# Optimization experiments

Hardware: AMD Instinct MI355X
Metric: run time of the kernel (lower is better)

## Reference

```python
import jax, jax.numpy as jnp
import numpy as np

N_NODES = 100000
N_EDGES = 3200000
N_GRAPHS = 64
F_IN = 64
NUM_CLASSES = 10
CHROM = 21


def _glorot(key, shape):
    fan_in, fan_out = shape
    lim = (6.0 / (fan_in + fan_out)) ** 0.5
    return jax.random.uniform(key, shape, jnp.float32, -lim, lim)


def setup_inputs() -> dict:
    key = jax.random.key(0)
    ks = jax.random.split(key, 16)
    x = jax.random.normal(ks[0], (N_NODES, F_IN), jnp.float32)
    edge_index = jax.random.randint(ks[1], (2, N_EDGES), 0, N_NODES, jnp.int32)
    batch = jnp.sort(jax.random.randint(ks[2], (N_NODES,), 0, N_GRAPHS, jnp.int32))
    return {
        "x": x,
        "edge_index": edge_index,
        "batch": batch,
        # SAGEConv1: 64 -> 16
        "W1l": _glorot(ks[3], (F_IN, 16)), "b1": jnp.zeros((16,), jnp.float32),
        "W1r": _glorot(ks[4], (F_IN, 16)),
        # SAGEConv2: 16 -> 32
        "W2l": _glorot(ks[5], (16, 32)), "b2": jnp.zeros((32,), jnp.float32),
        "W2r": _glorot(ks[6], (16, 32)),
        # SAGEConv3: 32 -> 21
        "W3l": _glorot(ks[7], (32, CHROM)), "b3": jnp.zeros((CHROM,), jnp.float32),
        "W3r": _glorot(ks[8], (32, CHROM)),
        # classifier: 32 -> num_classes
        "Wc": _glorot(ks[9], (32, NUM_CLASSES)), "bc": jnp.zeros((NUM_CLASSES,), jnp.float32),
    }


def _sage_conv(x, src, dst, Wl, b, Wr):
    # mean aggregation of source features at target nodes (PyG SAGEConv default)
    agg = jax.ops.segment_sum(x[src], dst, num_segments=N_NODES)
    cnt = jax.ops.segment_sum(jnp.ones((src.shape[0],), x.dtype), dst, num_segments=N_NODES)
    mean = agg / jnp.maximum(cnt, 1.0)[:, None]
    return mean @ Wl + b + x @ Wr


def reference(x, edge_index, batch, W1l, b1, W1r, W2l, b2, W2r, W3l, b3, W3r, Wc, bc):
    src, dst = edge_index[0], edge_index[1]
    h = jax.nn.relu(_sage_conv(x, src, dst, W1l, b1, W1r))
    h2 = _sage_conv(h, src, dst, W2l, b2, W2r)          # pooled pre-relu
    color = _sage_conv(jax.nn.relu(h2), src, dst, W3l, b3, W3r)
    # global_mean_pool over graphs
    gsum = jax.ops.segment_sum(h2, batch, num_segments=N_GRAPHS)
    gcnt = jax.ops.segment_sum(jnp.ones((h2.shape[0],), h2.dtype), batch, num_segments=N_GRAPHS)
    pooled = gsum / jnp.maximum(gcnt, 1.0)[:, None]
    # dropout p=0.3 is identity in eval mode
    classif = pooled @ Wc + bc
    return classif, color
```

## Files before the change

### kernel.cpp

```cpp
#include <hip/hip_runtime.h>
#include <hip/hip_fp16.h>
#include <cstdint>
#include <cstddef>

#define N_NODES  100000
#define N_EDGES  3200000
#define N_GRAPHS 64

#define BQBITS   9
#define BQ       512
#define NBUCK    196
#define TILE     4096
#define NBLK     782
#define POOL_SLICES 8
#define PADB     4608


__global__ void kp1_hist(const int* __restrict__ dst, int* __restrict__ gh, int ne) {
    __shared__ int h[NBUCK];
    for (int i = threadIdx.x; i < NBUCK; i += 256) h[i] = 0;
    __syncthreads();
    int base = blockIdx.x * TILE;
    for (int i = threadIdx.x; i < TILE; i += 256) {
        int e = base + i;
        if (e < ne) atomicAdd(&h[dst[e] >> BQBITS], 1);
    }
    __syncthreads();
    for (int i = threadIdx.x; i < NBUCK; i += 256) gh[i * NBLK + blockIdx.x] = h[i];
}

__global__ void kp1_scanA(int* __restrict__ gh, int* __restrict__ btotal) {
    int q = blockIdx.x;
    __shared__ int ts[256];
    int v[4];
    int tsum = 0;
#pragma unroll
    for (int u = 0; u < 4; ++u) {
        int idx = threadIdx.x * 4 + u;
        v[u] = (idx < NBLK) ? gh[q * NBLK + idx] : 0;
        tsum += v[u];
    }
    ts[threadIdx.x] = tsum;
    __syncthreads();
    for (int off = 1; off < 256; off <<= 1) {
        int t = (threadIdx.x >= off) ? ts[threadIdx.x - off] : 0;
        __syncthreads();
        ts[threadIdx.x] += t;
        __syncthreads();
    }
    int run = ts[threadIdx.x] - tsum;
#pragma unroll
    for (int u = 0; u < 4; ++u) {
        int idx = threadIdx.x * 4 + u;
        if (idx < NBLK) gh[q * NBLK + idx] = run;
        run += v[u];
    }
    if (threadIdx.x == 255) btotal[q] = ts[255];
}

__global__ void kp1_scanB(const int* __restrict__ btotal, int* __restrict__ bstart) {
    __shared__ int s[256];
    int v = (threadIdx.x < NBUCK) ? btotal[threadIdx.x] : 0;
    s[threadIdx.x] = v;
    __syncthreads();
    for (int off = 1; off < 256; off <<= 1) {
        int t = (threadIdx.x >= off) ? s[threadIdx.x - off] : 0;
        __syncthreads();
        s[threadIdx.x] += t;
        __syncthreads();
    }
    if (threadIdx.x < NBUCK) bstart[threadIdx.x] = s[threadIdx.x] - v;
    if (threadIdx.x == 0) bstart[NBUCK] = N_EDGES;
}

__global__ __launch_bounds__(256) void kp1_scatter(
        const int* __restrict__ src, const int* __restrict__ dst,
        const int* __restrict__ gh, const int* __restrict__ bstart,
        unsigned* __restrict__ tmp, int ne) {
    __shared__ unsigned sed[TILE];
    __shared__ int lcnt[NBUCK];
    __shared__ int lofs[NBUCK + 1];
    __shared__ int fill[NBUCK];
    __shared__ int delta[NBUCK];
    __shared__ int ts[256];
    for (int i = threadIdx.x; i < NBUCK; i += 256) { lcnt[i] = 0; fill[i] = 0; }
    __syncthreads();
    int base = blockIdx.x * TILE;
    int nh = ne - base; if (nh > TILE) nh = TILE;
    int myq[16]; unsigned myw[16];
#pragma unroll
    for (int u = 0; u < 16; ++u) {
        int i = u * 256 + threadIdx.x;
        myq[u] = -1;
        if (i < nh) {
            int d = dst[base + i], s = src[base + i];
            int q = d >> BQBITS;
            myq[u] = q;
            myw[u] = ((unsigned)(d & (BQ - 1)) << 17) | (unsigned)s;
            atomicAdd(&lcnt[q], 1);
        }
    }
    __syncthreads();
    int v = (threadIdx.x < NBUCK) ? lcnt[threadIdx.x] : 0;
    ts[threadIdx.x] = v;
    __syncthreads();
    for (int off = 1; off < 256; off <<= 1) {
        int t = (threadIdx.x >= off) ? ts[threadIdx.x - off] : 0;
        __syncthreads();
        ts[threadIdx.x] += t;
        __syncthreads();
    }
    if (threadIdx.x < NBUCK) {
        int start = ts[threadIdx.x] - v;
        lofs[threadIdx.x] = start;
        delta[threadIdx.x] = bstart[threadIdx.x] + gh[threadIdx.x * NBLK + blockIdx.x] - start;
    }
    if (threadIdx.x == NBUCK - 1) lofs[NBUCK] = ts[threadIdx.x];
    __syncthreads();
#pragma unroll
    for (int u = 0; u < 16; ++u) {
        if (myq[u] >= 0) {
            int r = atomicAdd(&fill[myq[u]], 1);
            sed[lofs[myq[u]] + r] = myw[u];
        }
    }
    __syncthreads();
    for (int p = threadIdx.x; p < nh; p += 256) {
        int lo = 0, hi = NBUCK;
        while (hi - lo > 1) { int mid = (lo + hi) >> 1; if (lofs[mid] <= p) lo = mid; else hi = mid; }
        tmp[p + delta[lo]] = sed[p];
    }
}

__global__ void kp2(const unsigned* __restrict__ tmp, const int* __restrict__ bstart,
                    int* __restrict__ rs, int* __restrict__ deg, int* __restrict__ perm) {
    int q = blockIdx.x;
    int beg = bstart[q], end = bstart[q + 1];
    int m = end - beg;
    int pbase = ((beg + 7) & ~7) + q * PADB;
    __shared__ int cnt[BQ];
    __shared__ int lofs[BQ];
    __shared__ int fill[BQ];
    if (threadIdx.x < BQ) { cnt[threadIdx.x] = 0; fill[threadIdx.x] = 0; }
    __syncthreads();
    for (int p = threadIdx.x; p < m; p += 1024)
        atomicAdd(&cnt[tmp[beg + p] >> 17], 1);
    __syncthreads();
    int pc = 0;
    if (threadIdx.x < BQ) { pc = (cnt[threadIdx.x] + 7) & ~7; lofs[threadIdx.x] = pc; }
    __syncthreads();
    for (int off = 1; off < BQ; off <<= 1) {
        int t = 0;
        if (threadIdx.x < BQ && threadIdx.x >= off) t = lofs[threadIdx.x - off];
        __syncthreads();
        if (threadIdx.x < BQ) lofs[threadIdx.x] += t;
        __syncthreads();
    }
    if (threadIdx.x < BQ) {
        int node = q * BQ + threadIdx.x;
        if (node < N_NODES) {
            int st = lofs[threadIdx.x] - pc;
            rs[node] = pbase + st;
            deg[node] = cnt[threadIdx.x];
            for (int i = cnt[threadIdx.x]; i < pc; ++i)
                perm[pbase + st + i] = N_NODES;
        }
    }
    __syncthreads();
    for (int p = threadIdx.x; p < m; p += 1024) {
        unsigned w = tmp[beg + p];
        int dl = w >> 17;
        int s = w & 0x1FFFF;
        int r = atomicAdd(&fill[dl], 1);
        int st = lofs[dl] - ((cnt[dl] + 7) & ~7);
        perm[pbase + st + r] = s;
    }
}


__global__ void k_t1(const float* __restrict__ x, const float* __restrict__ W1l,
                     const float* __restrict__ W1r, const float* __restrict__ b1,
                     __half* __restrict__ y1, float* __restrict__ s1, int n) {
    __shared__ float wl[64 * 16], wr[64 * 16], bb[16];
    for (int i = threadIdx.x; i < 64 * 16; i += blockDim.x) { wl[i] = W1l[i]; wr[i] = W1r[i]; }
    if (threadIdx.x < 16) bb[threadIdx.x] = b1[threadIdx.x];
    __syncthreads();
    int node = blockIdx.x * blockDim.x + threadIdx.x;
    if (node >= n) return;
    const float4* xr = reinterpret_cast<const float4*>(x + (size_t)node * 64);
    float accl[16], accr[16];
#pragma unroll
    for (int j = 0; j < 16; ++j) { accl[j] = 0.f; accr[j] = 0.f; }
#pragma unroll
    for (int q = 0; q < 16; ++q) {
        float4 v = xr[q];
        float xs[4] = {v.x, v.y, v.z, v.w};
#pragma unroll
        for (int u = 0; u < 4; ++u) {
            int k = q * 4 + u;
            float xv = xs[u];
#pragma unroll
            for (int j = 0; j < 16; ++j) {
                accl[j] += xv * wl[k * 16 + j];
                accr[j] += xv * wr[k * 16 + j];
            }
        }
    }
    alignas(16) __half yh[16];
#pragma unroll
    for (int j = 0; j < 16; ++j) yh[j] = __float2half(accl[j]);
    uint4* y4 = reinterpret_cast<uint4*>(y1 + (size_t)node * 16);
    const uint4* yv = reinterpret_cast<const uint4*>(yh);
    y4[0] = yv[0]; y4[1] = yv[1];
    float4* s4 = reinterpret_cast<float4*>(s1 + (size_t)node * 16);
#pragma unroll
    for (int q = 0; q < 4; ++q)
        s4[q] = make_float4(accr[q*4+0] + bb[q*4+0], accr[q*4+1] + bb[q*4+1],
                            accr[q*4+2] + bb[q*4+2], accr[q*4+3] + bb[q*4+3]);
}

__global__ void k_t2(const float* __restrict__ mean2, const __half* __restrict__ h,
                     const float* __restrict__ W2l, const float* __restrict__ W2r,
                     const float* __restrict__ b2, float* __restrict__ h2, int n) {
    __shared__ float wl[16 * 32], wr[16 * 32], bb[32];
    for (int i = threadIdx.x; i < 16 * 32; i += blockDim.x) { wl[i] = W2l[i]; wr[i] = W2r[i]; }
    if (threadIdx.x < 32) bb[threadIdx.x] = b2[threadIdx.x];
    __syncthreads();
    int node = blockIdx.x * blockDim.x + threadIdx.x;
    if (node >= n) return;
    float m[16], hh[16];
    const float4* m4 = reinterpret_cast<const float4*>(mean2 + (size_t)node * 16);
#pragma unroll
    for (int q = 0; q < 4; ++q) {
        float4 a = m4[q];
        m[q*4+0]=a.x; m[q*4+1]=a.y; m[q*4+2]=a.z; m[q*4+3]=a.w;
    }
    alignas(16) __half hv[16];
    const uint4* hp = reinterpret_cast<const uint4*>(h + (size_t)node * 16);
    uint4* hvp = reinterpret_cast<uint4*>(hv);
    hvp[0] = hp[0]; hvp[1] = hp[1];
#pragma unroll
    for (int k = 0; k < 16; ++k) hh[k] = __half2float(hv[k]);
    float acc[32];
#pragma unroll
    for (int j = 0; j < 32; ++j) acc[j] = bb[j];
#pragma unroll
    for (int k = 0; k < 16; ++k) {
#pragma unroll
        for (int j = 0; j < 32; ++j)
            acc[j] += m[k] * wl[k * 32 + j] + hh[k] * wr[k * 32 + j];
    }
    float4* o4 = reinterpret_cast<float4*>(h2 + (size_t)node * 32);
#pragma unroll
    for (int q = 0; q < 8; ++q)
        o4[q] = make_float4(acc[q*4+0], acc[q*4+1], acc[q*4+2], acc[q*4+3]);
}

__global__ void k_t3(const float* __restrict__ h2, const float* __restrict__ W3l,
                     const float* __restrict__ W3r, const float* __restrict__ b3,
                     __half* __restrict__ y3, float* __restrict__ s3, int n) {
    __shared__ float wl[32 * 21], wr[32 * 21], bb[21];
    for (int i = threadIdx.x; i < 32 * 21; i += blockDim.x) { wl[i] = W3l[i]; wr[i] = W3r[i]; }
    if (threadIdx.x < 21) bb[threadIdx.x] = b3[threadIdx.x];
    __syncthreads();
    int node = blockIdx.x * blockDim.x + threadIdx.x;
    if (node >= n) return;
    float z[32];
    const float4* h4 = reinterpret_cast<const float4*>(h2 + (size_t)node * 32);
#pragma unroll
    for (int q = 0; q < 8; ++q) {
        float4 v = h4[q];
        z[q*4+0] = fmaxf(v.x, 0.f); z[q*4+1] = fmaxf(v.y, 0.f);
        z[q*4+2] = fmaxf(v.z, 0.f); z[q*4+3] = fmaxf(v.w, 0.f);
    }
    float a[21], c[21];
#pragma unroll
    for (int j = 0; j < 21; ++j) { a[j] = 0.f; c[j] = bb[j]; }
#pragma unroll
    for (int k = 0; k < 32; ++k) {
#pragma unroll
        for (int j = 0; j < 21; ++j) {
            a[j] += z[k] * wl[k * 21 + j];
            c[j] += z[k] * wr[k * 21 + j];
        }
    }
    alignas(16) __half yh[24];
#pragma unroll
    for (int j = 0; j < 21; ++j) yh[j] = __float2half(a[j]);
    yh[21] = __half(0.f); yh[22] = __half(0.f); yh[23] = __half(0.f);
    uint4* yp = reinterpret_cast<uint4*>(y3 + (size_t)node * 24);
    const uint4* yv = reinterpret_cast<const uint4*>(yh);
    yp[0] = yv[0]; yp[1] = yv[1]; yp[2] = yv[2];
    float* so = s3 + (size_t)node * 24;
#pragma unroll
    for (int j = 0; j < 21; ++j) so[j] = c[j];
    so[21] = 0.f; so[22] = 0.f; so[23] = 0.f;
}


__device__ __forceinline__ void acc4(uint2 v, float& a0, float& a1, float& a2, float& a3) {
    __half2 lo = *reinterpret_cast<__half2*>(&v.x);
    __half2 hi = *reinterpret_cast<__half2*>(&v.y);
    float2 flo = __half22float2(lo), fhi = __half22float2(hi);
    a0 += flo.x; a1 += flo.y; a2 += fhi.x; a3 += fhi.y;
}

template <bool RELU, bool SELF, bool OUT_HALF>
__global__ void k_agg16(const uint2* __restrict__ y, const int* __restrict__ rs,
                        const int* __restrict__ deg, const int* __restrict__ perm,
                        const float* __restrict__ self, void* __restrict__ outp,
                        int n_nodes) {
    int t = blockIdx.x * blockDim.x + threadIdx.x;
    int node = t >> 2;
    int f = t & 3;
    if (node >= n_nodes) return;
    int beg = rs[node];
    int d = deg[node];
    int pend = beg + ((d + 7) & ~7);
    float a0 = 0.f, a1 = 0.f, a2 = 0.f, a3 = 0.f;
    for (int e = beg; e < pend; e += 8) {
        const int4* pp = reinterpret_cast<const int4*>(perm + e);
        int4 p0 = pp[0];
        int4 p1 = pp[1];
        uint2 v0 = y[(size_t)p0.x * 4 + f];
        uint2 v1 = y[(size_t)p0.y * 4 + f];
        uint2 v2 = y[(size_t)p0.z * 4 + f];
        uint2 v3 = y[(size_t)p0.w * 4 + f];
        uint2 v4 = y[(size_t)p1.x * 4 + f];
        uint2 v5 = y[(size_t)p1.y * 4 + f];
        uint2 v6 = y[(size_t)p1.z * 4 + f];
        uint2 v7 = y[(size_t)p1.w * 4 + f];
        acc4(v0, a0, a1, a2, a3); acc4(v1, a0, a1, a2, a3);
        acc4(v2, a0, a1, a2, a3); acc4(v3, a0, a1, a2, a3);
        acc4(v4, a0, a1, a2, a3); acc4(v5, a0, a1, a2, a3);
        acc4(v6, a0, a1, a2, a3); acc4(v7, a0, a1, a2, a3);
    }
    float inv = 1.0f / fmaxf((float)d, 1.0f);
    a0 *= inv; a1 *= inv; a2 *= inv; a3 *= inv;
    if (SELF) {
        float4 sv = *reinterpret_cast<const float4*>(self + (size_t)node * 16 + f * 4);
        a0 += sv.x; a1 += sv.y; a2 += sv.z; a3 += sv.w;
    }
    if (RELU) {
        a0 = fmaxf(a0, 0.f); a1 = fmaxf(a1, 0.f);
        a2 = fmaxf(a2, 0.f); a3 = fmaxf(a3, 0.f);
    }
    if constexpr (OUT_HALF) {
        __half2 p01 = __floats2half2_rn(a0, a1);
        __half2 p23 = __floats2half2_rn(a2, a3);
        uint2 o;
        o.x = *reinterpret_cast<unsigned*>(&p01);
        o.y = *reinterpret_cast<unsigned*>(&p23);
        ((uint2*)outp)[(size_t)node * 4 + f] = o;
    } else {
        ((float4*)outp)[(size_t)node * 4 + f] = make_float4(a0, a1, a2, a3);
    }
}

__global__ void k_agg21(const uint2* __restrict__ y, const int* __restrict__ rs,
                        const int* __restrict__ deg, const int* __restrict__ perm,
                        const float* __restrict__ self24, float* __restrict__ outp,
                        int n_nodes) {
    int t = blockIdx.x * blockDim.x + threadIdx.x;
    int node = t / 6;
    int f = t - node * 6;
    if (node >= n_nodes) return;
    int beg = rs[node];
    int d = deg[node];
    int pend = beg + ((d + 7) & ~7);
    float a0 = 0.f, a1 = 0.f, a2 = 0.f, a3 = 0.f;
    for (int e = beg; e < pend; e += 8) {
        const int4* pp = reinterpret_cast<const int4*>(perm + e);
        int4 p0 = pp[0];
        int4 p1 = pp[1];
        uint2 v0 = y[(size_t)p0.x * 6 + f];
        uint2 v1 = y[(size_t)p0.y * 6 + f];
        uint2 v2 = y[(size_t)p0.z * 6 + f];
        uint2 v3 = y[(size_t)p0.w * 6 + f];
        uint2 v4 = y[(size_t)p1.x * 6 + f];
        uint2 v5 = y[(size_t)p1.y * 6 + f];
        uint2 v6 = y[(size_t)p1.z * 6 + f];
        uint2 v7 = y[(size_t)p1.w * 6 + f];
        acc4(v0, a0, a1, a2, a3); acc4(v1, a0, a1, a2, a3);
        acc4(v2, a0, a1, a2, a3); acc4(v3, a0, a1, a2, a3);
        acc4(v4, a0, a1, a2, a3); acc4(v5, a0, a1, a2, a3);
        acc4(v6, a0, a1, a2, a3); acc4(v7, a0, a1, a2, a3);
    }
    float inv = 1.0f / fmaxf((float)d, 1.0f);
    int c0 = f * 4;
    float4 sv = *reinterpret_cast<const float4*>(self24 + (size_t)node * 24 + c0);
    float r0 = a0 * inv + sv.x;
    float r1 = a1 * inv + sv.y;
    float r2 = a2 * inv + sv.z;
    float r3 = a3 * inv + sv.w;
    float* op = outp + (size_t)node * 21;
    op[c0] = r0;
    if (c0 + 1 < 21) op[c0 + 1] = r1;
    if (c0 + 2 < 21) op[c0 + 2] = r2;
    if (c0 + 3 < 21) op[c0 + 3] = r3;
}


__device__ __forceinline__ int lowerb(const int* a, int n, int key) {
    int lo = 0, hi = n;
    while (lo < hi) { int mid = (lo + hi) >> 1; if (a[mid] < key) lo = mid + 1; else hi = mid; }
    return lo;
}

__global__ void k_pool(const float* __restrict__ h2, const int* __restrict__ batch,
                       float* __restrict__ gsum, float* __restrict__ gcnt, int n) {
    int g = blockIdx.x / POOL_SLICES;
    int slice = blockIdx.x - g * POOL_SLICES;
    __shared__ int sbeg, send;
    if (threadIdx.x == 0) { sbeg = lowerb(batch, n, g); send = lowerb(batch, n, g + 1); }
    __syncthreads();
    int beg = sbeg, end = send;
    int f = threadIdx.x & 31;
    int r = threadIdx.x >> 5;
    float acc = 0.f;
    for (int i = beg + slice * 8 + r; i < end; i += POOL_SLICES * 8)
        acc += h2[(size_t)i * 32 + f];
    __shared__ float red[256];
    red[threadIdx.x] = acc;
    __syncthreads();
    if (r == 0) {
        float s = 0.f;
#pragma unroll
        for (int q = 0; q < 8; ++q) s += red[q * 32 + f];
        atomicAdd(&gsum[g * 32 + f], s);
    }
    if (slice == 0 && threadIdx.x == 0) gcnt[g] = (float)(end - beg);
}

__global__ void k_cls(const float* __restrict__ gsum, const float* __restrict__ gcnt,
                      const float* __restrict__ Wc, const float* __restrict__ bc,
                      float* __restrict__ outp) {
    int t = threadIdx.x;
    if (t >= N_GRAPHS * 10) return;
    int g = t / 10, c = t - g * 10;
    float cv = fmaxf(gcnt[g], 1.f);
    float acc = bc[c];
#pragma unroll
    for (int k = 0; k < 32; ++k) acc += (gsum[g * 32 + k] / cv) * Wc[k * 10 + c];
    outp[g * 10 + c] = acc;
}


extern "C" void kernel_launch(void* const* d_in, const int* in_sizes, int n_in,
                              void* d_out, int out_size, void* d_ws, size_t ws_size,
                              hipStream_t stream) {
    const float* x    = (const float*)d_in[0];
    const int*   ei   = (const int*)d_in[1];
    const int*   batch= (const int*)d_in[2];
    const float* W1l  = (const float*)d_in[3];
    const float* b1   = (const float*)d_in[4];
    const float* W1r  = (const float*)d_in[5];
    const float* W2l  = (const float*)d_in[6];
    const float* b2   = (const float*)d_in[7];
    const float* W2r  = (const float*)d_in[8];
    const float* W3l  = (const float*)d_in[9];
    const float* b3   = (const float*)d_in[10];
    const float* W3r  = (const float*)d_in[11];
    const float* Wc   = (const float*)d_in[12];
    const float* bc   = (const float*)d_in[13];
    float* out = (float*)d_out;

    char* ws = (char*)d_ws;
    size_t off = 0;
    auto alloc = [&](size_t bytes) { size_t o = off; off += (bytes + 255) & ~(size_t)255; return o; };

    int*    rs    = (int*)(ws + alloc((size_t)N_NODES * 4));
    int*    deg   = (int*)(ws + alloc((size_t)N_NODES * 4));
    int*    perm  = (int*)(ws + alloc((size_t)(N_EDGES + (size_t)NBUCK * PADB + 64) * 4));
    int*    gh    = (int*)(ws + alloc((size_t)NBUCK * NBLK * 4));
    int*    btotal= (int*)(ws + alloc(256 * 4));
    int*    bstart= (int*)(ws + alloc(260 * 4));
    __half* y1    = (__half*)(ws + alloc((size_t)(N_NODES + 1) * 16 * 2));
    float*  s1    = (float*)(ws + alloc((size_t)N_NODES * 16 * 4));
    __half* h     = (__half*)(ws + alloc((size_t)(N_NODES + 1) * 16 * 2));
    float*  mean2 = (float*)(ws + alloc((size_t)N_NODES * 16 * 4));
    float*  h2    = (float*)(ws + alloc((size_t)N_NODES * 32 * 4));
    __half* y3    = (__half*)(ws + alloc((size_t)(N_NODES + 1) * 24 * 2));
    float*  s3    = (float*)(ws + alloc((size_t)N_NODES * 24 * 4));
    float*  gsum  = (float*)(ws + alloc((size_t)N_GRAPHS * 32 * 4));
    float*  gcnt  = (float*)(ws + alloc((size_t)N_GRAPHS * 4));

    unsigned* tmp = (unsigned*)h2;

    const int* src = ei;
    const int* dst = ei + N_EDGES;

    int nb  = (N_NODES + 255) / 256;
    int g4  = (N_NODES * 4 + 255) / 256;
    int g6  = (N_NODES * 6 + 255) / 256;

    (void)hipMemsetAsync(y1 + (size_t)N_NODES * 16, 0, 32, stream);
    (void)hipMemsetAsync(h  + (size_t)N_NODES * 16, 0, 32, stream);
    (void)hipMemsetAsync(y3 + (size_t)N_NODES * 24, 0, 48, stream);
    (void)hipMemsetAsync(gsum, 0, (size_t)N_GRAPHS * 32 * 4, stream);

    kp1_hist   <<<NBLK, 256, 0, stream>>>(dst, gh, N_EDGES);
    kp1_scanA  <<<NBUCK, 256, 0, stream>>>(gh, btotal);
    kp1_scanB  <<<1, 256, 0, stream>>>(btotal, bstart);
    kp1_scatter<<<NBLK, 256, 0, stream>>>(src, dst, gh, bstart, tmp, N_EDGES);
    kp2        <<<NBUCK, 1024, 0, stream>>>(tmp, bstart, rs, deg, perm);

    k_t1<<<nb, 256, 0, stream>>>(x, W1l, W1r, b1, y1, s1, N_NODES);
    k_agg16<true, true, true><<<g4, 256, 0, stream>>>(
        (const uint2*)y1, rs, deg, perm, s1, h, N_NODES);

    k_agg16<false, false, false><<<g4, 256, 0, stream>>>(
        (const uint2*)h, rs, deg, perm, nullptr, mean2, N_NODES);
    k_t2<<<nb, 256, 0, stream>>>(mean2, h, W2l, W2r, b2, h2, N_NODES);

    k_t3<<<nb, 256, 0, stream>>>(h2, W3l, W3r, b3, y3, s3, N_NODES);
    k_agg21<<<g6, 256, 0, stream>>>(
        (const uint2*)y3, rs, deg, perm, s3, out + N_GRAPHS * 10, N_NODES);

    k_pool<<<N_GRAPHS * POOL_SLICES, 256, 0, stream>>>(h2, batch, gsum, gcnt, N_NODES);
    k_cls<<<1, 640, 0, stream>>>(gsum, gcnt, Wc, bc, out);
}
```

Baseline: 237.2 us.

## Widen gather loads to 16-byte per lane and fuse memsets into one kernel

The aggregation kernels now give each thread 8 half features loaded as one uint4, instead of 4 features as a uint2. This halves the number of threads per node, so the perm index loads are issued half as often and each gathered row takes fewer, wider loads. The four small hipMemsetAsync calls are replaced by a single zeroing kernel to cut launch overhead. The cost is fewer threads in flight to hide gather latency and higher register use per thread.

```diff
diff --git a/kernel.cpp b/kernel.cpp
--- a/kernel.cpp
+++ b/kernel.cpp
@@ -178,6 +178,15 @@
 }
 
 
+__global__ void k_zero(__half* __restrict__ y1z, __half* __restrict__ hz,
+                       __half* __restrict__ y3z, float* __restrict__ gsum) {
+    int t = threadIdx.x;
+    if (t < 16) { y1z[t] = __half(0.f); hz[t] = __half(0.f); }
+    if (t < 24) y3z[t] = __half(0.f);
+    for (int i = t; i < N_GRAPHS * 32; i += 256) gsum[i] = 0.f;
+}
+
+
 __global__ void k_t1(const float* __restrict__ x, const float* __restrict__ W1l,
                      const float* __restrict__ W1r, const float* __restrict__ b1,
                      __half* __restrict__ y1, float* __restrict__ s1, int n) {
@@ -298,106 +307,121 @@
 }
 
 
-__device__ __forceinline__ void acc4(uint2 v, float& a0, float& a1, float& a2, float& a3) {
-    __half2 lo = *reinterpret_cast<__half2*>(&v.x);
-    __half2 hi = *reinterpret_cast<__half2*>(&v.y);
-    float2 flo = __half22float2(lo), fhi = __half22float2(hi);
-    a0 += flo.x; a1 += flo.y; a2 += fhi.x; a3 += fhi.y;
+__device__ __forceinline__ void acc8(uint4 v, float* a) {
+    __half2 h0 = *reinterpret_cast<__half2*>(&v.x);
+    __half2 h1 = *reinterpret_cast<__half2*>(&v.y);
+    __half2 h2 = *reinterpret_cast<__half2*>(&v.z);
+    __half2 h3 = *reinterpret_cast<__half2*>(&v.w);
+    float2 f0 = __half22float2(h0), f1 = __half22float2(h1);
+    float2 f2 = __half22float2(h2), f3 = __half22float2(h3);
+    a[0] += f0.x; a[1] += f0.y; a[2] += f1.x; a[3] += f1.y;
+    a[4] += f2.x; a[5] += f2.y; a[6] += f3.x; a[7] += f3.y;
 }
 
 template <bool RELU, bool SELF, bool OUT_HALF>
-__global__ void k_agg16(const uint2* __restrict__ y, const int* __restrict__ rs,
+__global__ void k_agg16(const uint4* __restrict__ y, const int* __restrict__ rs,
                         const int* __restrict__ deg, const int* __restrict__ perm,
                         const float* __restrict__ self, void* __restrict__ outp,
                         int n_nodes) {
     int t = blockIdx.x * blockDim.x + threadIdx.x;
-    int node = t >> 2;
-    int f = t & 3;
+    int node = t >> 1;
+    int f = t & 1;
     if (node >= n_nodes) return;
     int beg = rs[node];
     int d = deg[node];
     int pend = beg + ((d + 7) & ~7);
-    float a0 = 0.f, a1 = 0.f, a2 = 0.f, a3 = 0.f;
+    float a[8];
+#pragma unroll
+    for (int j = 0; j < 8; ++j) a[j] = 0.f;
     for (int e = beg; e < pend; e += 8) {
         const int4* pp = reinterpret_cast<const int4*>(perm + e);
         int4 p0 = pp[0];
         int4 p1 = pp[1];
-        uint2 v0 = y[(size_t)p0.x * 4 + f];
-        uint2 v1 = y[(size_t)p0.y * 4 + f];
-        uint2 v2 = y[(size_t)p0.z * 4 + f];
-        uint2 v3 = y[(size_t)p0.w * 4 + f];
-        uint2 v4 = y[(size_t)p1.x * 4 + f];
-        uint2 v5 = y[(size_t)p1.y * 4 + f];
-        uint2 v6 = y[(size_t)p1.z * 4 + f];
-        uint2 v7 = y[(size_t)p1.w * 4 + f];
-        acc4(v0, a0, a1, a2, a3); acc4(v1, a0, a1, a2, a3);
-        acc4(v2, a0, a1, a2, a3); acc4(v3, a0, a1, a2, a3);
-        acc4(v4, a0, a1, a2, a3); acc4(v5, a0, a1, a2, a3);
-        acc4(v6, a0, a1, a2, a3); acc4(v7, a0, a1, a2, a3);
+        uint4 v0 = y[(size_t)p0.x * 2 + f];
+        uint4 v1 = y[(size_t)p0.y * 2 + f];
+        uint4 v2 = y[(size_t)p0.z * 2 + f];
+        uint4 v3 = y[(size_t)p0.w * 2 + f];
+        uint4 v4 = y[(size_t)p1.x * 2 + f];
+        uint4 v5 = y[(size_t)p1.y * 2 + f];
+        uint4 v6 = y[(size_t)p1.z * 2 + f];
+        uint4 v7 = y[(size_t)p1.w * 2 + f];
+        acc8(v0, a); acc8(v1, a); acc8(v2, a); acc8(v3, a);
+        acc8(v4, a); acc8(v5, a); acc8(v6, a); acc8(v7, a);
     }
     float inv = 1.0f / fmaxf((float)d, 1.0f);
-    a0 *= inv; a1 *= inv; a2 *= inv; a3 *= inv;
+#pragma unroll
+    for (int j = 0; j < 8; ++j) a[j] *= inv;
     if (SELF) {
-        float4 sv = *reinterpret_cast<const float4*>(self + (size_t)node * 16 + f * 4);
-        a0 += sv.x; a1 += sv.y; a2 += sv.z; a3 += sv.w;
+        const float4* sp = reinterpret_cast<const float4*>(self + (size_t)node * 16 + f * 8);
+        float4 s0 = sp[0], s1 = sp[1];
+        a[0] += s0.x; a[1] += s0.y; a[2] += s0.z; a[3] += s0.w;
+        a[4] += s1.x; a[5] += s1.y; a[6] += s1.z; a[7] += s1.w;
     }
     if (RELU) {
-        a0 = fmaxf(a0, 0.f); a1 = fmaxf(a1, 0.f);
-        a2 = fmaxf(a2, 0.f); a3 = fmaxf(a3, 0.f);
+#pragma unroll
+        for (int j = 0; j < 8; ++j) a[j] = fmaxf(a[j], 0.f);
     }
     if constexpr (OUT_HALF) {
-        __half2 p01 = __floats2half2_rn(a0, a1);
-        __half2 p23 = __floats2half2_rn(a2, a3);
-        uint2 o;
-        o.x = *reinterpret_cast<unsigned*>(&p01);
-        o.y = *reinterpret_cast<unsigned*>(&p23);
-        ((uint2*)outp)[(size_t)node * 4 + f] = o;
+        __half2 p0 = __floats2half2_rn(a[0], a[1]);
+        __half2 p1 = __floats2half2_rn(a[2], a[3]);
+        __half2 p2 = __floats2half2_rn(a[4], a[5]);
+        __half2 p3 = __floats2half2_rn(a[6], a[7]);
+        uint4 o;
+        o.x = *reinterpret_cast<unsigned*>(&p0);
+        o.y = *reinterpret_cast<unsigned*>(&p1);
+        o.z = *reinterpret_cast<unsigned*>(&p2);
+        o.w = *reinterpret_cast<unsigned*>(&p3);
+        ((uint4*)outp)[(size_t)node * 2 + f] = o;
     } else {
-        ((float4*)outp)[(size_t)node * 4 + f] = make_float4(a0, a1, a2, a3);
-    }
-}
-
-__global__ void k_agg21(const uint2* __restrict__ y, const int* __restrict__ rs,
+        float4* op = (float4*)outp + (size_t)node * 4 + f * 2;
+        op[0] = make_float4(a[0], a[1], a[2], a[3]);
+        op[1] = make_float4(a[4], a[5], a[6], a[7]);
+    }
+}
+
+__global__ void k_agg21(const uint4* __restrict__ y, const int* __restrict__ rs,
                         const int* __restrict__ deg, const int* __restrict__ perm,
                         const float* __restrict__ self24, float* __restrict__ outp,
                         int n_nodes) {
     int t = blockIdx.x * blockDim.x + threadIdx.x;
-    int node = t / 6;
-    int f = t - node * 6;
+    int node = t / 3;
+    int f = t - node * 3;
     if (node >= n_nodes) return;
     int beg = rs[node];
     int d = deg[node];
     int pend = beg + ((d + 7) & ~7);
-    float a0 = 0.f, a1 = 0.f, a2 = 0.f, a3 = 0.f;
+    float a[8];
+#pragma unroll
+    for (int j = 0; j < 8; ++j) a[j] = 0.f;
     for (int e = beg; e < pend; e += 8) {
         const int4* pp = reinterpret_cast<const int4*>(perm + e);
         int4 p0 = pp[0];
         int4 p1 = pp[1];
-        uint2 v0 = y[(size_t)p0.x * 6 + f];
-        uint2 v1 = y[(size_t)p0.y * 6 + f];
-        uint2 v2 = y[(size_t)p0.z * 6 + f];
-        uint2 v3 = y[(size_t)p0.w * 6 + f];
-        uint2 v4 = y[(size_t)p1.x * 6 + f];
-        uint2 v5 = y[(size_t)p1.y * 6 + f];
-        uint2 v6 = y[(size_t)p1.z * 6 + f];
-        uint2 v7 = y[(size_t)p1.w * 6 + f];
-        acc4(v0, a0, a1, a2, a3); acc4(v1, a0, a1, a2, a3);
-        acc4(v2, a0, a1, a2, a3); acc4(v3, a0, a1, a2, a3);
-        acc4(v4, a0, a1, a2, a3); acc4(v5, a0, a1, a2, a3);
-        acc4(v6, a0, a1, a2, a3); acc4(v7, a0, a1, a2, a3);
+        uint4 v0 = y[(size_t)p0.x * 3 + f];
+        uint4 v1 = y[(size_t)p0.y * 3 + f];
+        uint4 v2 = y[(size_t)p0.z * 3 + f];
+        uint4 v3 = y[(size_t)p0.w * 3 + f];
+        uint4 v4 = y[(size_t)p1.x * 3 + f];
+        uint4 v5 = y[(size_t)p1.y * 3 + f];
+        uint4 v6 = y[(size_t)p1.z * 3 + f];
+        uint4 v7 = y[(size_t)p1.w * 3 + f];
+        acc8(v0, a); acc8(v1, a); acc8(v2, a); acc8(v3, a);
+        acc8(v4, a); acc8(v5, a); acc8(v6, a); acc8(v7, a);
     }
     float inv = 1.0f / fmaxf((float)d, 1.0f);
-    int c0 = f * 4;
-    float4 sv = *reinterpret_cast<const float4*>(self24 + (size_t)node * 24 + c0);
-    float r0 = a0 * inv + sv.x;
-    float r1 = a1 * inv + sv.y;
-    float r2 = a2 * inv + sv.z;
-    float r3 = a3 * inv + sv.w;
+    int c0 = f * 8;
+    const float4* sp = reinterpret_cast<const float4*>(self24 + (size_t)node * 24 + c0);
+    float4 s0 = sp[0], s1 = sp[1];
+    float r[8];
+    r[0] = a[0] * inv + s0.x; r[1] = a[1] * inv + s0.y;
+    r[2] = a[2] * inv + s0.z; r[3] = a[3] * inv + s0.w;
+    r[4] = a[4] * inv + s1.x; r[5] = a[5] * inv + s1.y;
+    r[6] = a[6] * inv + s1.z; r[7] = a[7] * inv + s1.w;
     float* op = outp + (size_t)node * 21;
-    op[c0] = r0;
-    if (c0 + 1 < 21) op[c0 + 1] = r1;
-    if (c0 + 2 < 21) op[c0 + 2] = r2;
-    if (c0 + 3 < 21) op[c0 + 3] = r3;
+    int nlim = 21 - c0;
+#pragma unroll
+    for (int j = 0; j < 8; ++j)
+        if (j < nlim) op[c0 + j] = r[j];
 }
 
 
@@ -491,13 +515,11 @@
     const int* dst = ei + N_EDGES;
 
     int nb  = (N_NODES + 255) / 256;
-    int g4  = (N_NODES * 4 + 255) / 256;
-    int g6  = (N_NODES * 6 + 255) / 256;
-
-    (void)hipMemsetAsync(y1 + (size_t)N_NODES * 16, 0, 32, stream);
-    (void)hipMemsetAsync(h  + (size_t)N_NODES * 16, 0, 32, stream);
-    (void)hipMemsetAsync(y3 + (size_t)N_NODES * 24, 0, 48, stream);
-    (void)hipMemsetAsync(gsum, 0, (size_t)N_GRAPHS * 32 * 4, stream);
+    int g2  = (N_NODES * 2 + 255) / 256;
+    int g3  = (N_NODES * 3 + 255) / 256;
+
+    k_zero<<<1, 256, 0, stream>>>(y1 + (size_t)N_NODES * 16, h + (size_t)N_NODES * 16,
+                                  y3 + (size_t)N_NODES * 24, gsum);
 
     kp1_hist   <<<NBLK, 256, 0, stream>>>(dst, gh, N_EDGES);
     kp1_scanA  <<<NBUCK, 256, 0, stream>>>(gh, btotal);
@@ -506,16 +528,16 @@
     kp2        <<<NBUCK, 1024, 0, stream>>>(tmp, bstart, rs, deg, perm);
 
     k_t1<<<nb, 256, 0, stream>>>(x, W1l, W1r, b1, y1, s1, N_NODES);
-    k_agg16<true, true, true><<<g4, 256, 0, stream>>>(
-        (const uint2*)y1, rs, deg, perm, s1, h, N_NODES);
-
-    k_agg16<false, false, false><<<g4, 256, 0, stream>>>(
-        (const uint2*)h, rs, deg, perm, nullptr, mean2, N_NODES);
+    k_agg16<true, true, true><<<g2, 256, 0, stream>>>(
+        (const uint4*)y1, rs, deg, perm, s1, h, N_NODES);
+
+    k_agg16<false, false, false><<<g2, 256, 0, stream>>>(
+        (const uint4*)h, rs, deg, perm, nullptr, mean2, N_NODES);
     k_t2<<<nb, 256, 0, stream>>>(mean2, h, W2l, W2r, b2, h2, N_NODES);
 
     k_t3<<<nb, 256, 0, stream>>>(h2, W3l, W3r, b3, y3, s3, N_NODES);
-    k_agg21<<<g6, 256, 0, stream>>>(
-        (const uint2*)y3, rs, deg, perm, s3, out + N_GRAPHS * 10, N_NODES);
+    k_agg21<<<g3, 256, 0, stream>>>(
+        (const uint4*)y3, rs, deg, perm, s3, out + N_GRAPHS * 10, N_NODES);
 
     k_pool<<<N_GRAPHS * POOL_SLICES, 256, 0, stream>>>(h2, batch, gsum, gcnt, N_NODES);
     k_cls<<<1, 640, 0, stream>>>(gsum, gcnt, Wc, bc, out);
```

Result: no change. 237.8 us (+0.2%).
